# Optimization experiments

Measured on AMD Instinct MI355X. Metric: run time of the kernel, lower is better.

The kernel has to match this reference:

```python
import jax, jax.numpy as jnp
import numpy as np

# ---- static config (mirrors init_kwargs) ----
H, N, HKV = 32, 64, 8
HN = H * N            # model dim 2048
KV_DIM = HKV * N      # 512
B, T = 2, 1024
EPS = 1e-6
ROPE_THETA = 1.0e6
SPLITS_WAVGK = (96, 96, 64, 256, 64)   # xw, xa, xv, xg, xk lora ranks
SPLITS_RKV = (HN, KV_DIM, KV_DIM)


def rms_norm(x, w, eps=EPS):
    xf = x.astype(jnp.float32)
    var = jnp.mean(xf * xf, axis=-1, keepdims=True)
    return (w * (xf * jax.lax.rsqrt(var + eps))).astype(x.dtype)


def rotate_half(x):
    x1, x2 = jnp.split(x, 2, axis=-1)
    return jnp.concatenate((-x2, x1), axis=-1)


def apply_rope(q, k, cos, sin):
    # q:[B,T,H,N], k:[B,T,HKV,N], cos/sin:[B,T,N] -> unsqueeze head dim (unsqueeze_dim=2)
    cos = cos[:, :, None, :]
    sin = sin[:, :, None, :]
    return q * cos + rotate_half(q) * sin, k * cos + rotate_half(k) * sin


def rwkv7_recurrence(r, gk, k, v, a, b, S0):
    # fused_recurrent_rwkv7 (head_first=False). All inputs [B,T,H,N] fp32, S0 [B,H,N_key,N_val].
    # S_t = diag(exp(gk_t)) S_{t-1} + b_t (a_t^T S_{t-1}) + k_t v_t^T ;  o_t = r_t^T S_t
    def step(S, inp):
        r_t, w_t, k_t, v_t, a_t, b_t = inp
        sa = jnp.einsum('bhk,bhkv->bhv', a_t, S)
        S = (jnp.exp(w_t)[..., None] * S
             + k_t[..., None] * v_t[..., None, :]
             + b_t[..., None] * sa[..., None, :])
        o = jnp.einsum('bhk,bhkv->bhv', r_t, S)
        return S, o
    xs = tuple(jnp.swapaxes(t, 0, 1) for t in (r, gk, k, v, a, b))  # [T,B,H,N]
    S, o = jax.lax.scan(step, S0, xs)
    return jnp.swapaxes(o, 0, 1), S


def setup_inputs() -> dict:
    key = jax.random.key(0)
    ks = jax.random.split(key, 24)
    f32 = jnp.float32
    rn = lambda k, shape, s=1.0: jax.random.normal(k, shape, dtype=f32) * s

    x_in = rn(ks[0], (B, T, HN))
    v_first = rn(ks[1], (B, T, HKV, N))
    k_first = rn(ks[2], (B, T, HKV, N))
    state = jnp.zeros((B, H, N, N), f32)

    # real rope cache (faithful to get_batch_rope_cache output) at positions 0..T-1
    inv_freq = 1.0 / (ROPE_THETA ** (np.arange(0, N, 2, dtype=np.float32) / N))
    freqs = np.outer(np.arange(T, dtype=np.float32), inv_freq)  # [T, N/2]
    emb = np.concatenate([freqs, freqs], axis=-1)               # [T, N]
    calc_cos = jnp.broadcast_to(jnp.asarray(np.cos(emb), dtype=np.float32), (B, T, N))
    calc_sin = jnp.broadcast_to(jnp.asarray(np.sin(emb), dtype=np.float32), (B, T, N))

    wavgk1 = rn(ks[3], (HN, sum(SPLITS_WAVGK)), 0.02)
    w0 = rn(ks[4], (HN,), 0.5)
    w2 = rn(ks[5], (SPLITS_WAVGK[0], HN), 0.02)
    a0 = rn(ks[6], (HN,), 0.1)
    a2 = rn(ks[7], (SPLITS_WAVGK[1], HN), 0.02)
    v0 = rn(ks[8], (KV_DIM,), 0.1)
    v2 = rn(ks[9], (SPLITS_WAVGK[2], KV_DIM), 0.02)
    g2 = rn(ks[10], (SPLITS_WAVGK[3], HN), 0.02)
    k0 = rn(ks[11], (KV_DIM,), 0.1)
    k2 = rn(ks[12], (SPLITS_WAVGK[4], KV_DIM), 0.02)
    r_k = rn(ks[13], (H, N), 0.1)
    RKV = rn(ks[14], (HN, HN + 2 * KV_DIM), 0.02)   # fpx weight, dequantized form
    O = rn(ks[15], (HN, HN), 0.02)
    R_bias = rn(ks[16], (HN,), 0.02)
    K_bias = rn(ks[17], (KV_DIM,), 0.02)
    V_bias = rn(ks[18], (KV_DIM,), 0.02)
    ln_r = jnp.ones((N,), f32)
    ln_k = jnp.ones((N,), f32)
    ln1 = jnp.ones((HN,), f32)
    ln2 = jnp.ones((HN,), f32)

    return dict(x_in=x_in, v_first=v_first, k_first=k_first, state=state,
                calc_cos=calc_cos, calc_sin=calc_sin, wavgk1=wavgk1,
                w0=w0, w2=w2, a0=a0, a2=a2, v0=v0, v2=v2, g2=g2, k0=k0, k2=k2,
                r_k=r_k, RKV=RKV, O=O, R_bias=R_bias, K_bias=K_bias, V_bias=V_bias,
                ln_r=ln_r, ln_k=ln_k, ln1=ln1, ln2=ln2)


def reference(x_in, v_first, k_first, state, calc_cos, calc_sin, wavgk1,
              w0, w2, a0, a2, v0, v2, g2, k0, k2, r_k, RKV, O,
              R_bias, K_bias, V_bias, ln_r, ln_k, ln1, ln2):
    Bx, Tx, C = x_in.shape
    kv_repeat = HN // KV_DIM  # GQA repeat factor (4)

    x = rms_norm(x_in, ln1)
    xw, xa, xv, xg, xk = jnp.split(x @ wavgk1, np.cumsum(SPLITS_WAVGK)[:-1].tolist(), axis=-1)

    rkv = x @ RKV  # fpx_matmul -> dense matmul on dequantized weight
    r, k, v = jnp.split(rkv, np.cumsum(SPLITS_RKV)[:-1].tolist(), axis=-1)
    r = (r + R_bias).reshape(Bx, Tx, H, N)
    k = (k + K_bias).reshape(Bx, Tx, HKV, N)
    v = (v + V_bias).reshape(Bx, Tx, HKV, N)

    r = rms_norm(r, ln_r)
    k = rms_norm(k, ln_k)
    r, k = apply_rope(r, k, calc_cos, calc_sin)

    # layer_id = 1 (> 0): mix with first-layer value/key
    v = v + (v_first - v) * jax.nn.sigmoid(xv @ v2 + v0).reshape(Bx, Tx, HKV, N)
    k = k + (k_first - k) * jax.nn.sigmoid(xk @ k2 + k0).reshape(Bx, Tx, HKV, N)

    # repeat_kv: [B,T,HKV,N] -> [B,T,H,N] -> [B,T,HN]
    k = jnp.repeat(k, kv_repeat, axis=2).reshape(Bx, Tx, HN)
    v = jnp.repeat(v, kv_repeat, axis=2).reshape(Bx, Tx, HN)

    a = jax.nn.sigmoid(xa @ a2 + a0)  # in-context learning rate gate [B,T,HN]
    k4 = k.reshape(Bx, Tx, H, N)
    kk = (k4 / jnp.maximum(jnp.linalg.norm(k4, axis=-1, keepdims=True), 1e-12)).reshape(Bx, Tx, HN)

    w_log = -jax.nn.softplus(-(jnp.tanh(xw) @ w2 + w0)) - 0.5  # log-decay, <= -0.5
    k = k * (1.0 - w_log + a)
    aa = -kk
    bb = kk * a
    gk = -jnp.exp(w_log.astype(jnp.float32))  # passed to fused_recurrent_rwkv7 as log decay

    shp = (Bx, Tx, H, N)
    o, state_out = rwkv7_recurrence(
        r.reshape(shp).astype(jnp.float32), gk.reshape(shp),
        k.reshape(shp).astype(jnp.float32), v.reshape(shp).astype(jnp.float32),
        aa.reshape(shp).astype(jnp.float32), bb.reshape(shp).astype(jnp.float32),
        state.astype(jnp.float32))

    xx = o.reshape(Bx, Tx, HN) * (float(N) ** -0.5)
    bonus = ((r * k.reshape(shp) * r_k).sum(axis=-1, keepdims=True) * v.reshape(shp)).reshape(Bx, Tx, HN)
    xx = xx.astype(x_in.dtype) + bonus

    out = (xx * (jax.nn.sigmoid(xg) @ g2)) @ O  # fpx output projection
    x_new = x_in + out
    return rms_norm(x_new, ln2)
```

## Files before the change

### kernel.cpp

```cpp
#include <hip/hip_runtime.h>

typedef unsigned short u16;
typedef unsigned int u32;

using f32x4 = __attribute__((ext_vector_type(4))) float;
using bf16x8 = __attribute__((ext_vector_type(8))) __bf16;

#define HN 2048
#define KVD 512
#define TOKENS 2048
#define N1 3712
#define K2W 576
#define N2 7168

#define OFF_Y1   0ull
#define OFF_OO   0ull
#define OFF_XG   16777216ull
#define OFF_Y2   30408704ull
#define OFF_OUTR 30408704ull
#define OFF_BT1  89128960ull
#define OFF_XB   104333312ull
#define OFF_W2T  89128960ull
#define OFF_X2   97386496ull
#define OFF_OT   89128960ull
#define OFF_RR   112721920ull
#define OFF_DEC  129499136ull
#define OFF_KR   146276352ull
#define OFF_VV   163053568ull
#define OFF_AA   179830784ull
#define OFF_BB   196608000ull
#define WS_NEED  213385216ull

__device__ __forceinline__ u16 f2bf(float f) {
    u32 u = __float_as_uint(f);
    u32 r = u + 0x7fffu + ((u >> 16) & 1u);
    return (u16)(r >> 16);
}
__device__ __forceinline__ float sigm(float x) { return 1.f / (1.f + expf(-x)); }
__device__ __forceinline__ float wsum(float v) {
#pragma unroll
    for (int m = 32; m > 0; m >>= 1) v += __shfl_xor(v, m, 64);
    return v;
}
__device__ __forceinline__ float rowsum16(float v) {
    float t;
    t = __uint_as_float(__builtin_amdgcn_update_dpp(0, __float_as_uint(v), 0x121, 0xf, 0xf, true));
    v += t;
    t = __uint_as_float(__builtin_amdgcn_update_dpp(0, __float_as_uint(v), 0x122, 0xf, 0xf, true));
    v += t;
    t = __uint_as_float(__builtin_amdgcn_update_dpp(0, __float_as_uint(v), 0x124, 0xf, 0xf, true));
    v += t;
    t = __uint_as_float(__builtin_amdgcn_update_dpp(0, __float_as_uint(v), 0x128, 0xf, 0xf, true));
    v += t;
    return v;
}

typedef __attribute__((address_space(1))) const void glob_t;
typedef __attribute__((address_space(3))) void lds_t;
__device__ __forceinline__ void gload_lds16(const void* g, void* l) {
    __builtin_amdgcn_global_load_lds((glob_t*)g, (lds_t*)l, 16, 0, 0);
}

__global__ __launch_bounds__(256) void k_prep_bt1(const float* __restrict__ wavgk1,
                                                  const float* __restrict__ RKV,
                                                  u16* __restrict__ BT1) {
    __shared__ float tile[64][65];
    const int bn = blockIdx.x >> 5;
    const int bk = blockIdx.x & 31;
    const int n0 = bn << 6, k0 = bk << 6;
    const int c = threadIdx.x & 63, q = threadIdx.x >> 6;
#pragma unroll
    for (int i = 0; i < 16; ++i) {
        const int r = (q << 4) + i;
        float v = 0.f;
        if (bn < 9)       v = wavgk1[(size_t)(k0 + r) * 576 + n0 + c];
        else if (bn < 57) v = RKV[(size_t)(k0 + r) * 3072 + (n0 + c - 576)];
        tile[r][c] = v;
    }
    __syncthreads();
#pragma unroll
    for (int i = 0; i < 16; ++i) {
        const int rw = (q << 4) + i;
        BT1[(size_t)(n0 + rw) * 2048 + k0 + c] = f2bf(tile[c][rw]);
    }
}

__global__ __launch_bounds__(256) void k_prep_w2t(const float* __restrict__ w2, const float* __restrict__ a2,
                                                  const float* __restrict__ g2, const float* __restrict__ v2,
                                                  const float* __restrict__ k2, u16* __restrict__ W2T) {
    int idx = blockIdx.x * 256 + threadIdx.x;
    int n = idx / 576, c = idx - n * 576;
    float v = 0.f;
    if (n < 2048)      { if (c < 96)              v = w2[(size_t)c * 2048 + n]; }
    else if (n < 4096) { if (c >= 96 && c < 192)  v = a2[(size_t)(c - 96) * 2048 + (n - 2048)]; }
    else if (n < 6144) { if (c >= 192 && c < 448) v = g2[(size_t)(c - 192) * 2048 + (n - 4096)]; }
    else if (n < 6656) { if (c >= 448 && c < 512) v = v2[(size_t)(c - 448) * 512 + (n - 6144)]; }
    else               { if (c >= 512)            v = k2[(size_t)(c - 512) * 512 + (n - 6656)]; }
    W2T[idx] = f2bf(v);
}

__global__ __launch_bounds__(256) void k_prep_ot(const float* __restrict__ O, u16* __restrict__ OT) {
    __shared__ float tile[64][65];
    const int bn = blockIdx.x >> 5, bk = blockIdx.x & 31;
    const int n0 = bn << 6, k0 = bk << 6;
    const int c = threadIdx.x & 63, q = threadIdx.x >> 6;
#pragma unroll
    for (int i = 0; i < 16; ++i) {
        const int r = (q << 4) + i;
        tile[r][c] = O[(size_t)(k0 + r) * 2048 + n0 + c];
    }
    __syncthreads();
#pragma unroll
    for (int i = 0; i < 16; ++i) {
        const int rw = (q << 4) + i;
        OT[(size_t)(n0 + rw) * 2048 + k0 + c] = f2bf(tile[c][rw]);
    }
}

__global__ __launch_bounds__(256) void k_rms1(const float* __restrict__ X,
                                              const float* __restrict__ ln1,
                                              u16* __restrict__ XB) {
    const int t = blockIdx.x, tid = threadIdx.x;
    const float* row = X + ((size_t)t << 11);
    float4 v0 = *(const float4*)(row + tid * 8);
    float4 v1 = *(const float4*)(row + tid * 8 + 4);
    float ss = v0.x*v0.x + v0.y*v0.y + v0.z*v0.z + v0.w*v0.w
             + v1.x*v1.x + v1.y*v1.y + v1.z*v1.z + v1.w*v1.w;
    ss = wsum(ss);
    __shared__ float red[4];
    if ((tid & 63) == 0) red[tid >> 6] = ss;
    __syncthreads();
    float scale = rsqrtf((red[0] + red[1] + red[2] + red[3]) * (1.f / 2048.f) + 1e-6f);
    float4 w0_ = *(const float4*)(ln1 + tid * 8);
    float4 w1_ = *(const float4*)(ln1 + tid * 8 + 4);
    u16* o = XB + ((size_t)t << 11) + tid * 8;
    o[0] = f2bf(v0.x * scale * w0_.x); o[1] = f2bf(v0.y * scale * w0_.y);
    o[2] = f2bf(v0.z * scale * w0_.z); o[3] = f2bf(v0.w * scale * w0_.w);
    o[4] = f2bf(v1.x * scale * w1_.x); o[5] = f2bf(v1.y * scale * w1_.y);
    o[6] = f2bf(v1.z * scale * w1_.z); o[7] = f2bf(v1.w * scale * w1_.w);
}

__global__ __launch_bounds__(256) void k_gemm(const u16* __restrict__ A,
                                              const u16* __restrict__ Bt,
                                              float* __restrict__ C,
                                              int M, int N, int K) {
    __shared__ __align__(16) u16 tA[4096];
    __shared__ __align__(16) u16 tB[4096];
    const int tid = threadIdx.x;
    const int w = tid >> 6, l = tid & 63;
    const int bm = blockIdx.x << 7, bn = blockIdx.y << 7;
    const int wm = (w >> 1) << 6, wn = (w & 1) << 6;
    const int lrow = l >> 2;
    const int lk = (((l & 3) ^ ((l >> 3) & 3)) << 3);
    f32x4 acc[4][4] = {};
    const size_t rA0 = (size_t)(bm + (w << 4) + lrow) * K;
    const size_t rA1 = (size_t)(bm + ((w + 4) << 4) + lrow) * K;
    const size_t rB0 = (size_t)(bn + (w << 4) + lrow) * K;
    const size_t rB1 = (size_t)(bn + ((w + 4) << 4) + lrow) * K;
    const int frow = l & 15;
    const int koff = (((l >> 4) ^ ((l >> 1) & 3)) << 3);
    for (int kt = 0; kt < K; kt += 32) {
        gload_lds16(A + rA0 + kt + lk, &tA[w << 9]);
        gload_lds16(A + rA1 + kt + lk, &tA[2048 + (w << 9)]);
        gload_lds16(Bt + rB0 + kt + lk, &tB[w << 9]);
        gload_lds16(Bt + rB1 + kt + lk, &tB[2048 + (w << 9)]);
        __syncthreads();
        bf16x8 av[4], bv[4];
#pragma unroll
        for (int i = 0; i < 4; ++i) {
            av[i] = *(const bf16x8*)&tA[((wm + (i << 4) + frow) << 5) + koff];
            bv[i] = *(const bf16x8*)&tB[((wn + (i << 4) + frow) << 5) + koff];
        }
#pragma unroll
        for (int i = 0; i < 4; ++i)
#pragma unroll
            for (int j = 0; j < 4; ++j)
                acc[i][j] = __builtin_amdgcn_mfma_f32_16x16x32_bf16(av[i], bv[j], acc[i][j], 0, 0, 0);
        __syncthreads();
    }
    const int crow = bm + wm + ((l >> 4) << 2);
    const int ccol = bn + wn + (l & 15);
#pragma unroll
    for (int i = 0; i < 4; ++i)
#pragma unroll
        for (int j = 0; j < 4; ++j)
#pragma unroll
            for (int jj = 0; jj < 4; ++jj)
                C[(size_t)(crow + (i << 4) + jj) * N + ccol + (j << 4)] = acc[i][j][jj];
}

__global__ __launch_bounds__(256) void k_gemm2(const u16* __restrict__ A,
                                               const u16* __restrict__ Bt,
                                               float* __restrict__ C) {
    __shared__ __align__(16) u16 tA[4096];
    __shared__ __align__(16) u16 tB[4096];
    const int tid = threadIdx.x;
    const int w = tid >> 6, l = tid & 63;
    const int by = blockIdx.y;
    int c0, K;
    if (by < 16)      { c0 = 0;   K = 96; }
    else if (by < 32) { c0 = 96;  K = 96; }
    else if (by < 48) { c0 = 192; K = 256; }
    else if (by < 52) { c0 = 448; K = 64; }
    else              { c0 = 512; K = 64; }
    const int n0 = by << 7;
    const int bm = blockIdx.x << 7;
    const int wm = (w >> 1) << 6, wn = (w & 1) << 6;
    const int lrow = l >> 2;
    const int lk = (((l & 3) ^ ((l >> 3) & 3)) << 3);
    f32x4 acc[4][4] = {};
    const size_t rA0 = (size_t)(bm + (w << 4) + lrow) * 576 + c0;
    const size_t rA1 = (size_t)(bm + ((w + 4) << 4) + lrow) * 576 + c0;
    const size_t rB0 = (size_t)(n0 + (w << 4) + lrow) * 576 + c0;
    const size_t rB1 = (size_t)(n0 + ((w + 4) << 4) + lrow) * 576 + c0;
    const int frow = l & 15;
    const int koff = (((l >> 4) ^ ((l >> 1) & 3)) << 3);
    for (int kt = 0; kt < K; kt += 32) {
        gload_lds16(A + rA0 + kt + lk, &tA[w << 9]);
        gload_lds16(A + rA1 + kt + lk, &tA[2048 + (w << 9)]);
        gload_lds16(Bt + rB0 + kt + lk, &tB[w << 9]);
        gload_lds16(Bt + rB1 + kt + lk, &tB[2048 + (w << 9)]);
        __syncthreads();
        bf16x8 av[4], bv[4];
#pragma unroll
        for (int i = 0; i < 4; ++i) {
            av[i] = *(const bf16x8*)&tA[((wm + (i << 4) + frow) << 5) + koff];
            bv[i] = *(const bf16x8*)&tB[((wn + (i << 4) + frow) << 5) + koff];
        }
#pragma unroll
        for (int i = 0; i < 4; ++i)
#pragma unroll
            for (int j = 0; j < 4; ++j)
                acc[i][j] = __builtin_amdgcn_mfma_f32_16x16x32_bf16(av[i], bv[j], acc[i][j], 0, 0, 0);
        __syncthreads();
    }
    const int crow = bm + wm + ((l >> 4) << 2);
    const int ccol = n0 + wn + (l & 15);
#pragma unroll
    for (int i = 0; i < 4; ++i)
#pragma unroll
        for (int j = 0; j < 4; ++j)
#pragma unroll
            for (int jj = 0; jj < 4; ++jj)
                C[(size_t)(crow + (i << 4) + jj) * N2 + ccol + (j << 4)] = acc[i][j][jj];
}

__global__ __launch_bounds__(256) void k_prep_x2(const float* __restrict__ Y1, u16* __restrict__ X2) {
    int idx = blockIdx.x * 256 + threadIdx.x;
    int t = idx / 576, c = idx - t * 576;
    const float* y1 = Y1 + (size_t)t * N1;
    float v;
    if (c < 96)       v = tanhf(y1[c]);
    else if (c < 192) v = y1[c];
    else if (c < 448) v = sigm(y1[c + 64]);
    else if (c < 512) v = y1[c - 256];
    else              v = y1[c];
    X2[idx] = f2bf(v);
}

__global__ __launch_bounds__(256) void k_prep_rec(
    const float* __restrict__ Y1, const float* __restrict__ Y2,
    const float* __restrict__ v_first, const float* __restrict__ k_first,
    const float* __restrict__ cosb, const float* __restrict__ sinb,
    const float* __restrict__ w0, const float* __restrict__ a0,
    const float* __restrict__ v0b, const float* __restrict__ k0b,
    const float* __restrict__ R_bias, const float* __restrict__ K_bias,
    const float* __restrict__ V_bias, const float* __restrict__ ln_r,
    const float* __restrict__ ln_k,
    float* __restrict__ RR, float* __restrict__ DEC, float* __restrict__ KR,
    float* __restrict__ VV, float* __restrict__ AA, float* __restrict__ BB) {
    const int t = blockIdx.x, tid = threadIdx.x;
    const int ww = tid >> 6, lane = tid & 63;
    const float* y1 = Y1 + (size_t)t * N1;
    const float* y2 = Y2 + (size_t)t * N2;
    const float cs = cosb[t * 64 + lane];
    const float sn = sinb[t * 64 + lane];
    const float sign = lane < 32 ? -1.f : 1.f;
    const size_t tb = (size_t)t << 11;
    __shared__ float kkv[512], vkv[512];
#pragma unroll
    for (int i = 0; i < 8; ++i) {
        int h = ww * 8 + i, c = h * 64 + lane;
        float rr = y1[576 + c] + R_bias[c];
        float ssq = wsum(rr * rr);
        float rn = ln_r[lane] * rr * rsqrtf(ssq * (1.f / 64.f) + 1e-6f);
        float rot = sign * __shfl(rn, lane ^ 32, 64);
        RR[tb + c] = rn * cs + rot * sn;
    }
#pragma unroll
    for (int i = 0; i < 2; ++i) {
        int j = ww * 2 + i, c = j * 64 + lane;
        float kr = y1[2624 + c] + K_bias[c];
        float ssq = wsum(kr * kr);
        float kn = ln_k[lane] * kr * rsqrtf(ssq * (1.f / 64.f) + 1e-6f);
        float rot = sign * __shfl(kn, lane ^ 32, 64);
        float krope = kn * cs + rot * sn;
        float ksig = sigm(y2[6656 + c] + k0b[c]);
        kkv[c] = krope + (k_first[(size_t)t * 512 + c] - krope) * ksig;
        float vr = y1[3136 + c] + V_bias[c];
        float vsig = sigm(y2[6144 + c] + v0b[c]);
        vkv[c] = vr + (v_first[(size_t)t * 512 + c] - vr) * vsig;
    }
    __syncthreads();
#pragma unroll
    for (int i = 0; i < 8; ++i) {
        int h = ww * 8 + i, c = h * 64 + lane;
        int ckv = (h >> 2) * 64 + lane;
        float kb = kkv[ckv], vb = vkv[ckv];
        float a_ = sigm(y2[2048 + c] + a0[c]);
        float wr = y2[c] + w0[c];
        float z = -wr;
        float sp = fmaxf(z, 0.f) + log1pf(expf(-fabsf(z)));
        float w_log = -sp - 0.5f;
        float ssq = wsum(kb * kb);
        float kk = kb / fmaxf(sqrtf(ssq), 1e-12f);
        DEC[tb + c] = expf(-expf(w_log));
        KR[tb + c] = kb * (1.f - w_log + a_);
        VV[tb + c] = vb;
        AA[tb + c] = -kk;
        BB[tb + c] = kk * a_;
    }
}

__global__ __launch_bounds__(256, 1) void k_recv10(
    const float* __restrict__ RRp, const float* __restrict__ DECp,
    const float* __restrict__ KRp, const float* __restrict__ VVp,
    const float* __restrict__ AAp, const float* __restrict__ BBp,
    const float* __restrict__ S0, float* __restrict__ OO) {
    __shared__ __align__(16) float cbuf[2][6][32][64];
    const int tid = threadIdx.x;
    const int wl = tid >> 6;
    const int lane = tid & 63;
    const int vl = lane >> 4;
    const int kq = lane & 15;
    const int quarter = blockIdx.x & 3;
    const int ch = blockIdx.x >> 2;
    const int vcol = (quarter << 4) + (wl << 2) + vl;
    const size_t cb = ((size_t)(ch >> 5) * 1024 * 2048) + ((size_t)(ch & 31) << 6);

    const float* s0 = S0 + ((size_t)ch << 12);
    float L0 = s0[((kq << 2) + 0) * 64 + vcol];
    float L1 = s0[((kq << 2) + 1) * 64 + vcol];
    float L2 = s0[((kq << 2) + 2) * 64 + vcol];
    float L3 = s0[((kq << 2) + 3) * 64 + vcol];

    const float* gsrc[6] = {AAp, DECp, KRp, BBp, RRp, VVp};
    const int trow = (wl << 2) + vl;

#define STG(B, T0)                                                             \
    {                                                                          \
        const size_t g0 = cb + (size_t)((T0) + trow) * 2048 + (kq << 2);       \
        const size_t g1 = cb + (size_t)((T0) + 16 + trow) * 2048 + (kq << 2);  \
        float* lb = &cbuf[B][0][0][0] + (wl << 8);                             \
        _Pragma("unroll") for (int ar = 0; ar < 6; ++ar) {                     \
            gload_lds16(gsrc[ar] + g0, lb + ar * 2048);                        \
            gload_lds16(gsrc[ar] + g1, lb + ar * 2048 + 1024);                 \
        }                                                                      \
    }

#define LDC(P, S)                                                              \
    A4 = *(const float4*)((P) + ((S) << 6) + (kq << 2));                       \
    D4 = *(const float4*)((P) + 2048 + ((S) << 6) + (kq << 2));                \
    K4 = *(const float4*)((P) + 4096 + ((S) << 6) + (kq << 2));                \
    B4 = *(const float4*)((P) + 6144 + ((S) << 6) + (kq << 2));                \
    R4 = *(const float4*)((P) + 8192 + ((S) << 6) + (kq << 2));                \
    Vs = (P)[10240 + ((S) << 6) + vcol];

    STG(0, 0);
    __syncthreads();

    float4 A4, D4, K4, B4, R4;
    float Vs;
    {
        const float* bp0 = &cbuf[0][0][0][0];
        LDC(bp0, 0);
    }

    for (int c = 0; c < 32; ++c) {
        const int b = c & 1;
        if (c < 31) STG(b ^ 1, (c + 1) << 5);
        const float* cp = &cbuf[b][0][0][0];
#pragma unroll 4
        for (int s = 0; s < 32; ++s) {
            const int sn = (s + 1) & 31;
            const int so = sn << 6;
            const float4 nA = *(const float4*)(cp + so + (kq << 2));
            const float4 nD = *(const float4*)(cp + 2048 + so + (kq << 2));
            const float4 nK = *(const float4*)(cp + 4096 + so + (kq << 2));
            const float4 nB = *(const float4*)(cp + 6144 + so + (kq << 2));
            const float4 nR = *(const float4*)(cp + 8192 + so + (kq << 2));
            const float  nV = cp[10240 + so + vcol];
            float sp = fmaf(L1, A4.y, L0 * A4.x) + fmaf(L3, A4.w, L2 * A4.z);
            const float sa = rowsum16(sp);
            L0 = fmaf(B4.x, sa, fmaf(K4.x, Vs, L0 * D4.x));
            L1 = fmaf(B4.y, sa, fmaf(K4.y, Vs, L1 * D4.y));
            L2 = fmaf(B4.z, sa, fmaf(K4.z, Vs, L2 * D4.z));
            L3 = fmaf(B4.w, sa, fmaf(K4.w, Vs, L3 * D4.w));
            float op = fmaf(L1, R4.y, L0 * R4.x) + fmaf(L3, R4.w, L2 * R4.z);
            const float o = rowsum16(op);
            if (kq == 0) OO[cb + ((size_t)((c << 5) + s) << 11) + vcol] = o;
            A4 = nA; D4 = nD; K4 = nK; B4 = nB; R4 = nR; Vs = nV;
        }
        __syncthreads();
        if (c < 31) {
            const float* np = &cbuf[b ^ 1][0][0][0];
            LDC(np, 0);
        }
    }
#undef LDC
#undef STG
}

__global__ __launch_bounds__(256) void k_gate(
    const float* __restrict__ OOp, const float* __restrict__ RRp,
    const float* __restrict__ KRp, const float* __restrict__ VVp,
    const float* __restrict__ Y2, const float* __restrict__ r_k,
    u16* __restrict__ XG) {
    const int t = blockIdx.x, tid = threadIdx.x;
    const int ww = tid >> 6, lane = tid & 63;
    const size_t tb = (size_t)t << 11;
#pragma unroll
    for (int i = 0; i < 8; ++i) {
        int c = (ww * 8 + i) * 64 + lane;
        float pr = RRp[tb + c] * KRp[tb + c] * r_k[c];
        float dot = wsum(pr);
        float xx = OOp[tb + c] * 0.125f + dot * VVp[tb + c];
        float g = Y2[(size_t)t * N2 + 4096 + c];
        XG[tb + c] = f2bf(xx * g);
    }
}

__global__ __launch_bounds__(256) void k_final(const float* __restrict__ x_in,
                                               const float* __restrict__ OUTR,
                                               const float* __restrict__ ln2,
                                               float* __restrict__ out) {
    const int t = blockIdx.x, tid = threadIdx.x;
    const float* xr = x_in + ((size_t)t << 11);
    const float* orow = OUTR + ((size_t)t << 11);
    float4 a0 = *(const float4*)(xr + tid * 8);
    float4 a1 = *(const float4*)(xr + tid * 8 + 4);
    float4 b0 = *(const float4*)(orow + tid * 8);
    float4 b1 = *(const float4*)(orow + tid * 8 + 4);
    float v[8] = {a0.x + b0.x, a0.y + b0.y, a0.z + b0.z, a0.w + b0.w,
                  a1.x + b1.x, a1.y + b1.y, a1.z + b1.z, a1.w + b1.w};
    float ss = 0.f;
#pragma unroll
    for (int i = 0; i < 8; ++i) ss = fmaf(v[i], v[i], ss);
    ss = wsum(ss);
    __shared__ float red[4];
    if ((tid & 63) == 0) red[tid >> 6] = ss;
    __syncthreads();
    float scale = rsqrtf((red[0] + red[1] + red[2] + red[3]) * (1.f / 2048.f) + 1e-6f);
    float* o = out + ((size_t)t << 11) + tid * 8;
#pragma unroll
    for (int i = 0; i < 8; ++i) o[i] = ln2[tid * 8 + i] * v[i] * scale;
}

extern "C" void kernel_launch(void* const* d_in, const int* in_sizes, int n_in,
                              void* d_out, int out_size, void* d_ws, size_t ws_size,
                              hipStream_t stream) {
    const float* x_in    = (const float*)d_in[0];
    const float* v_first = (const float*)d_in[1];
    const float* k_first = (const float*)d_in[2];
    const float* state   = (const float*)d_in[3];
    const float* cosb    = (const float*)d_in[4];
    const float* sinb    = (const float*)d_in[5];
    const float* wavgk1  = (const float*)d_in[6];
    const float* w0      = (const float*)d_in[7];
    const float* w2      = (const float*)d_in[8];
    const float* a0      = (const float*)d_in[9];
    const float* a2      = (const float*)d_in[10];
    const float* v0      = (const float*)d_in[11];
    const float* v2      = (const float*)d_in[12];
    const float* g2      = (const float*)d_in[13];
    const float* k0      = (const float*)d_in[14];
    const float* k2      = (const float*)d_in[15];
    const float* r_k     = (const float*)d_in[16];
    const float* RKV     = (const float*)d_in[17];
    const float* O       = (const float*)d_in[18];
    const float* R_bias  = (const float*)d_in[19];
    const float* K_bias  = (const float*)d_in[20];
    const float* V_bias  = (const float*)d_in[21];
    const float* ln_r    = (const float*)d_in[22];
    const float* ln_k    = (const float*)d_in[23];
    const float* ln1     = (const float*)d_in[24];
    const float* ln2     = (const float*)d_in[25];

    if (ws_size < WS_NEED) return;

    char* ws = (char*)d_ws;
    u16*   BT1  = (u16*)(ws + OFF_BT1);
    u16*   W2T  = (u16*)(ws + OFF_W2T);
    u16*   OT   = (u16*)(ws + OFF_OT);
    u16*   XB   = (u16*)(ws + OFF_XB);
    float* Y1   = (float*)(ws + OFF_Y1);
    u16*   X2   = (u16*)(ws + OFF_X2);
    float* Y2   = (float*)(ws + OFF_Y2);
    float* RR   = (float*)(ws + OFF_RR);
    float* DEC  = (float*)(ws + OFF_DEC);
    float* KR   = (float*)(ws + OFF_KR);
    float* VV   = (float*)(ws + OFF_VV);
    float* AA   = (float*)(ws + OFF_AA);
    float* BB   = (float*)(ws + OFF_BB);
    float* OO   = (float*)(ws + OFF_OO);
    u16*   XG   = (u16*)(ws + OFF_XG);
    float* OUTR = (float*)(ws + OFF_OUTR);

    k_prep_bt1<<<1856, 256, 0, stream>>>(wavgk1, RKV, BT1);
    k_rms1<<<2048, 256, 0, stream>>>(x_in, ln1, XB);
    k_gemm<<<dim3(16, 29), 256, 0, stream>>>(XB, BT1, Y1, 2048, N1, 2048);
    k_prep_w2t<<<16128, 256, 0, stream>>>(w2, a2, g2, v2, k2, W2T);
    k_prep_x2<<<4608, 256, 0, stream>>>(Y1, X2);
    k_gemm2<<<dim3(16, 56), 256, 0, stream>>>(X2, W2T, Y2);
    k_prep_rec<<<2048, 256, 0, stream>>>(Y1, Y2, v_first, k_first, cosb, sinb,
                                         w0, a0, v0, k0, R_bias, K_bias, V_bias,
                                         ln_r, ln_k, RR, DEC, KR, VV, AA, BB);
    k_prep_ot<<<1024, 256, 0, stream>>>(O, OT);
    k_recv10<<<256, 256, 0, stream>>>(RR, DEC, KR, VV, AA, BB, state, OO);
    k_gate<<<2048, 256, 0, stream>>>(OO, RR, KR, VV, Y2, r_k, XG);
    k_gemm<<<dim3(16, 16), 256, 0, stream>>>(XG, OT, OUTR, 2048, 2048, 2048);
    k_final<<<2048, 256, 0, stream>>>(x_in, OUTR, ln2, (float*)d_out);
}
```

Baseline: 401.1 us.

## Reformulate recurrence output to shorten per-step dependency chain

Result: slower. 419.9 us (+4.7%).

```diff
diff --git a/kernel.cpp b/kernel.cpp
--- a/kernel.cpp
+++ b/kernel.cpp
@@ -29,7 +29,9 @@
 #define OFF_VV   163053568ull
 #define OFF_AA   179830784ull
 #define OFF_BB   196608000ull
-#define WS_NEED  213385216ull
+#define OFF_RKB  213385216ull
+#define OFF_RD   213909504ull
+#define WS_NEED  230686720ull
 
 __device__ __forceinline__ u16 f2bf(float f) {
     u32 u = __float_as_uint(f);
@@ -268,7 +270,8 @@
     const float* __restrict__ V_bias, const float* __restrict__ ln_r,
     const float* __restrict__ ln_k,
     float* __restrict__ RR, float* __restrict__ DEC, float* __restrict__ KR,
-    float* __restrict__ VV, float* __restrict__ AA, float* __restrict__ BB) {
+    float* __restrict__ VV, float* __restrict__ AA, float* __restrict__ BB,
+    float* __restrict__ RD, float* __restrict__ RKB) {
     const int t = blockIdx.x, tid = threadIdx.x;
     const int ww = tid >> 6, lane = tid & 63;
     const float* y1 = Y1 + (size_t)t * N1;
@@ -278,6 +281,7 @@
     const float sign = lane < 32 ? -1.f : 1.f;
     const size_t tb = (size_t)t << 11;
     __shared__ float kkv[512], vkv[512];
+    float rsave[8];
 #pragma unroll
     for (int i = 0; i < 8; ++i) {
         int h = ww * 8 + i, c = h * 64 + lane;
@@ -285,7 +289,8 @@
         float ssq = wsum(rr * rr);
         float rn = ln_r[lane] * rr * rsqrtf(ssq * (1.f / 64.f) + 1e-6f);
         float rot = sign * __shfl(rn, lane ^ 32, 64);
-        RR[tb + c] = rn * cs + rot * sn;
+        rsave[i] = rn * cs + rot * sn;
+        RR[tb + c] = rsave[i];
     }
 #pragma unroll
     for (int i = 0; i < 2; ++i) {
@@ -314,20 +319,34 @@
         float w_log = -sp - 0.5f;
         float ssq = wsum(kb * kb);
         float kk = kb / fmaxf(sqrtf(ssq), 1e-12f);
-        DEC[tb + c] = expf(-expf(w_log));
-        KR[tb + c] = kb * (1.f - w_log + a_);
+        const float dec = expf(-expf(w_log));
+        const float kr2 = kb * (1.f - w_log + a_);
+        const float bb2 = kk * a_;
+        const float rrv = rsave[i];
+        DEC[tb + c] = dec;
+        KR[tb + c] = kr2;
         VV[tb + c] = vb;
         AA[tb + c] = -kk;
-        BB[tb + c] = kk * a_;
-    }
-}
-
-__global__ __launch_bounds__(256, 1) void k_recv10(
-    const float* __restrict__ RRp, const float* __restrict__ DECp,
-    const float* __restrict__ KRp, const float* __restrict__ VVp,
-    const float* __restrict__ AAp, const float* __restrict__ BBp,
+        BB[tb + c] = bb2;
+        RD[tb + c] = rrv * dec;
+        const float rk = wsum(rrv * kr2);
+        const float rb = wsum(rrv * bb2);
+        if (lane == 0) {
+            const int chain = (t >> 10) * 32 + h;
+            RKB[(size_t)chain * 2048 + ((t & 1023) << 1)] = rk;
+            RKB[(size_t)chain * 2048 + ((t & 1023) << 1) + 1] = rb;
+        }
+    }
+}
+
+__global__ __launch_bounds__(256, 1) void k_recv11(
+    const float* __restrict__ DECp, const float* __restrict__ KRp,
+    const float* __restrict__ VVp, const float* __restrict__ AAp,
+    const float* __restrict__ BBp, const float* __restrict__ RDp,
+    const float* __restrict__ RKBp,
     const float* __restrict__ S0, float* __restrict__ OO) {
     __shared__ __align__(16) float cbuf[2][6][32][64];
+    __shared__ float tailb[2][64];
     const int tid = threadIdx.x;
     const int wl = tid >> 6;
     const int lane = tid & 63;
@@ -344,7 +363,7 @@
     float L2 = s0[((kq << 2) + 2) * 64 + vcol];
     float L3 = s0[((kq << 2) + 3) * 64 + vcol];
 
-    const float* gsrc[6] = {AAp, DECp, KRp, BBp, RRp, VVp};
+    const float* gsrc[6] = {AAp, DECp, KRp, BBp, RDp, VVp};
     const int trow = (wl << 2) + vl;
 
 #define STG(B, T0)                                                             \
@@ -356,30 +375,35 @@
             gload_lds16(gsrc[ar] + g0, lb + ar * 2048);                        \
             gload_lds16(gsrc[ar] + g1, lb + ar * 2048 + 1024);                 \
         }                                                                      \
-    }
-
-#define LDC(P, S)                                                              \
+        if (wl == 0)                                                           \
+            tailb[B][lane] = RKBp[(size_t)ch * 2048 + ((T0) << 1) + lane];     \
+    }
+
+#define LDC(P, TL, S)                                                          \
     A4 = *(const float4*)((P) + ((S) << 6) + (kq << 2));                       \
     D4 = *(const float4*)((P) + 2048 + ((S) << 6) + (kq << 2));                \
     K4 = *(const float4*)((P) + 4096 + ((S) << 6) + (kq << 2));                \
     B4 = *(const float4*)((P) + 6144 + ((S) << 6) + (kq << 2));                \
     R4 = *(const float4*)((P) + 8192 + ((S) << 6) + (kq << 2));                \
-    Vs = (P)[10240 + ((S) << 6) + vcol];
+    Vs = (P)[10240 + ((S) << 6) + vcol];                                       \
+    RK2 = *(const float2*)((TL) + ((S) << 1));
 
     STG(0, 0);
     __syncthreads();
 
     float4 A4, D4, K4, B4, R4;
     float Vs;
+    float2 RK2;
     {
         const float* bp0 = &cbuf[0][0][0][0];
-        LDC(bp0, 0);
+        LDC(bp0, &tailb[0][0], 0);
     }
 
     for (int c = 0; c < 32; ++c) {
         const int b = c & 1;
         if (c < 31) STG(b ^ 1, (c + 1) << 5);
         const float* cp = &cbuf[b][0][0][0];
+        const float* tl = &tailb[b][0];
 #pragma unroll 4
         for (int s = 0; s < 32; ++s) {
             const int sn = (s + 1) & 31;
@@ -390,21 +414,23 @@
             const float4 nB = *(const float4*)(cp + 6144 + so + (kq << 2));
             const float4 nR = *(const float4*)(cp + 8192 + so + (kq << 2));
             const float  nV = cp[10240 + so + vcol];
+            const float2 nRK = *(const float2*)(tl + (sn << 1));
             float sp = fmaf(L1, A4.y, L0 * A4.x) + fmaf(L3, A4.w, L2 * A4.z);
+            float od = fmaf(L1, R4.y, L0 * R4.x) + fmaf(L3, R4.w, L2 * R4.z);
             const float sa = rowsum16(sp);
+            const float odr = rowsum16(od);
             L0 = fmaf(B4.x, sa, fmaf(K4.x, Vs, L0 * D4.x));
             L1 = fmaf(B4.y, sa, fmaf(K4.y, Vs, L1 * D4.y));
             L2 = fmaf(B4.z, sa, fmaf(K4.z, Vs, L2 * D4.z));
             L3 = fmaf(B4.w, sa, fmaf(K4.w, Vs, L3 * D4.w));
-            float op = fmaf(L1, R4.y, L0 * R4.x) + fmaf(L3, R4.w, L2 * R4.z);
-            const float o = rowsum16(op);
+            const float o = odr + fmaf(RK2.x, Vs, RK2.y * sa);
             if (kq == 0) OO[cb + ((size_t)((c << 5) + s) << 11) + vcol] = o;
-            A4 = nA; D4 = nD; K4 = nK; B4 = nB; R4 = nR; Vs = nV;
+            A4 = nA; D4 = nD; K4 = nK; B4 = nB; R4 = nR; Vs = nV; RK2 = nRK;
         }
         __syncthreads();
         if (c < 31) {
             const float* np = &cbuf[b ^ 1][0][0][0];
-            LDC(np, 0);
+            LDC(np, &tailb[b ^ 1][0], 0);
         }
     }
 #undef LDC
@@ -502,6 +528,8 @@
     float* VV   = (float*)(ws + OFF_VV);
     float* AA   = (float*)(ws + OFF_AA);
     float* BB   = (float*)(ws + OFF_BB);
+    float* RKB  = (float*)(ws + OFF_RKB);
+    float* RD   = (float*)(ws + OFF_RD);
     float* OO   = (float*)(ws + OFF_OO);
     u16*   XG   = (u16*)(ws + OFF_XG);
     float* OUTR = (float*)(ws + OFF_OUTR);
@@ -514,9 +542,9 @@
     k_gemm2<<<dim3(16, 56), 256, 0, stream>>>(X2, W2T, Y2);
     k_prep_rec<<<2048, 256, 0, stream>>>(Y1, Y2, v_first, k_first, cosb, sinb,
                                          w0, a0, v0, k0, R_bias, K_bias, V_bias,
-                                         ln_r, ln_k, RR, DEC, KR, VV, AA, BB);
+                                         ln_r, ln_k, RR, DEC, KR, VV, AA, BB, RD, RKB);
     k_prep_ot<<<1024, 256, 0, stream>>>(O, OT);
-    k_recv10<<<256, 256, 0, stream>>>(RR, DEC, KR, VV, AA, BB, state, OO);
+    k_recv11<<<256, 256, 0, stream>>>(DEC, KR, VV, AA, BB, RD, RKB, state, OO);
     k_gate<<<2048, 256, 0, stream>>>(OO, RR, KR, VV, Y2, r_k, XG);
     k_gemm<<<dim3(16, 16), 256, 0, stream>>>(XG, OT, OUTR, 2048, 2048, 2048);
     k_final<<<2048, 256, 0, stream>>>(x_in, OUTR, ln2, (float*)d_out);
```
